# Kernel optimization log

Hardware: AMD Instinct MI355X
Metric: run time of the kernel (lower is better)

Reference implementation:

```python
import jax, jax.numpy as jnp
import numpy as np

B, L, D_MODEL = 8, 256, 256
D_STATE, D_INNER, DT_RANK, D_CONV = 16, 512, 16, 4


def _ln(x, g, b, eps):
    mu = x.mean(-1, keepdims=True)
    var = ((x - mu) ** 2).mean(-1, keepdims=True)
    return (x - mu) * jax.lax.rsqrt(var + eps) * g + b


def _ssm(x, W_in, conv_w, conv_b, W_x, W_dt, b_dt, A_log, Dp, W_out):
    # x: (B, L, D_MODEL) -- standard Mamba selective-scan block
    xz = x @ W_in                                  # (B,L,2*Di)
    xc, z = jnp.split(xz, 2, axis=-1)
    K = conv_w.shape[-1]
    xp = jnp.pad(xc, ((0, 0), (K - 1, 0), (0, 0)))  # causal depthwise conv
    xc = sum(xp[:, k:k + L, :] * conv_w[:, k] for k in range(K)) + conv_b
    xc = jax.nn.silu(xc)
    x_dbl = xc @ W_x                               # (B,L,R+2S)
    dt, Bm, Cm = jnp.split(x_dbl, [DT_RANK, DT_RANK + D_STATE], axis=-1)
    dt = jax.nn.softplus(dt @ W_dt + b_dt)         # (B,L,Di)
    A = -jnp.exp(A_log)                            # (Di,S)
    dA = jnp.exp(dt[..., None] * A)                # (B,L,Di,S)
    dBx = dt[..., None] * Bm[:, :, None, :] * xc[..., None]

    def step(h, inp):
        dA_t, dBx_t, C_t = inp
        h = dA_t * h + dBx_t                       # (B,Di,S)
        y = jnp.einsum('bds,bs->bd', h, C_t)
        return h, y

    h0 = jnp.zeros((xc.shape[0], D_INNER, D_STATE), xc.dtype)
    xs = (dA.transpose(1, 0, 2, 3), dBx.transpose(1, 0, 2, 3), Cm.transpose(1, 0, 2))
    _, ys = jax.lax.scan(step, h0, xs)             # (L,B,Di)
    y = ys.transpose(1, 0, 2) + xc * Dp
    y = y * jax.nn.silu(z)
    return y @ W_out


def _basic(x, ln_g, ln_b, ssm_params):
    # Basic_Block: ReLU(SSM(LN(x))) + x  (drop_path=0, attn_drop=0)
    return jax.nn.relu(_ssm(_ln(x, ln_g, ln_b, 1e-6), *ssm_params)) + x


def setup_inputs() -> dict:
    key = jax.random.key(0)
    ks = jax.random.split(key, 32)

    def n(k, shape, s=0.02):
        return jax.random.normal(k, shape, dtype=jnp.float32) * s

    inp = {}
    inp['x_spa'] = jax.random.normal(ks[0], (B, L, D_MODEL), dtype=jnp.float32)
    inp['x_spe'] = jax.random.normal(ks[1], (B, L, D_MODEL), dtype=jnp.float32)
    i = 2
    A_init = jnp.log(jnp.tile(jnp.arange(1, D_STATE + 1, dtype=jnp.float32), (D_INNER, 1)))
    for p in ('spa', 'spe'):
        inp[p + '_ln_g'] = jnp.ones((D_MODEL,), jnp.float32)
        inp[p + '_ln_b'] = jnp.zeros((D_MODEL,), jnp.float32)
        inp[p + '_W_in'] = n(ks[i], (D_MODEL, 2 * D_INNER)); i += 1
        inp[p + '_conv_w'] = n(ks[i], (D_INNER, D_CONV), 0.1); i += 1
        inp[p + '_conv_b'] = jnp.zeros((D_INNER,), jnp.float32)
        inp[p + '_W_x'] = n(ks[i], (D_INNER, DT_RANK + 2 * D_STATE)); i += 1
        inp[p + '_W_dt'] = n(ks[i], (DT_RANK, D_INNER), 0.1); i += 1
        inp[p + '_b_dt'] = n(ks[i], (D_INNER,), 0.1); i += 1
        inp[p + '_A_log'] = A_init
        inp[p + '_D'] = jnp.ones((D_INNER,), jnp.float32)
        inp[p + '_W_out'] = n(ks[i], (D_INNER, D_MODEL)); i += 1
    inp['sc_W'] = n(ks[i], (D_MODEL, D_MODEL)); i += 1
    inp['sc_b'] = jnp.zeros((D_MODEL,), jnp.float32)
    inp['sc_ln_g'] = jnp.ones((D_MODEL,), jnp.float32)
    inp['sc_ln_b'] = jnp.zeros((D_MODEL,), jnp.float32)
    inp['fusion_W'] = n(ks[i], (D_MODEL, D_MODEL))
    return inp


def reference(x_spa, x_spe,
              spa_ln_g, spa_ln_b, spa_W_in, spa_conv_w, spa_conv_b, spa_W_x,
              spa_W_dt, spa_b_dt, spa_A_log, spa_D, spa_W_out,
              spe_ln_g, spe_ln_b, spe_W_in, spe_conv_w, spe_conv_b, spe_W_x,
              spe_W_dt, spe_b_dt, spe_A_log, spe_D, spe_W_out,
              sc_W, sc_b, sc_ln_g, sc_ln_b, fusion_W):
    # shared shortcut: Linear + LayerNorm (eps=1e-5)
    ident_spa = _ln(x_spa @ sc_W + sc_b, sc_ln_g, sc_ln_b, 1e-5)
    ident_spe = _ln(x_spe @ sc_W + sc_b, sc_ln_g, sc_ln_b, 1e-5)
    spa_p = (spa_W_in, spa_conv_w, spa_conv_b, spa_W_x, spa_W_dt, spa_b_dt, spa_A_log, spa_D, spa_W_out)
    spe_p = (spe_W_in, spe_conv_w, spe_conv_b, spe_W_x, spe_W_dt, spe_b_dt, spe_A_log, spe_D, spe_W_out)
    a = _basic(x_spa, spa_ln_g, spa_ln_b, spa_p)
    e = _basic(x_spe, spe_ln_g, spe_ln_b, spe_p)
    # fusion gate: mean-pool both branches, Linear(no bias) + sigmoid, broadcast-mul
    fw = jax.nn.sigmoid(((a.mean(1) + e.mean(1)) * 0.5) @ fusion_W)[:, None, :]
    a = a * fw
    e = e * fw
    return (a + ident_spa, e + ident_spe)
```

## Files before the change

kernel.cpp:

```cpp
#include <hip/hip_runtime.h>
#include <hip/hip_bf16.h>
#include <math.h>

#define BD 8
#define LD 256
#define DM 256
#define DS 16
#define DI 512
#define RK 16

#define NROWS (2*BD*LD)
#define HALF_ROWS (BD*LD)

typedef __attribute__((ext_vector_type(8))) short bhalf8;
typedef __attribute__((ext_vector_type(4))) float f32x4;

__device__ __forceinline__ float siluf(float x){ return x / (1.f + __expf(-x)); }
__device__ __forceinline__ float softplusf(float x){
  return fmaxf(x, 0.f) + log1pf(__expf(-fabsf(x)));
}
__device__ __forceinline__ unsigned short f2bf(float f){
  __hip_bfloat16 h = __float2bfloat16(f);
  return *reinterpret_cast<unsigned short*>(&h);
}

__global__ __launch_bounds__(256) void k_transpose(
    const float* __restrict__ Wi_spa, const float* __restrict__ Wi_spe,
    const float* __restrict__ Wo_spa, const float* __restrict__ Wo_spe,
    const float* __restrict__ scW,
    const float* __restrict__ Wx_spa, const float* __restrict__ Wx_spe,
    unsigned short* __restrict__ Wt_i_spa, unsigned short* __restrict__ Wt_i_spe,
    unsigned short* __restrict__ Wt_o_spa, unsigned short* __restrict__ Wt_o_spe,
    unsigned short* __restrict__ scWt,
    unsigned short* __restrict__ Wxt_spa, unsigned short* __restrict__ Wxt_spe)
{
  __shared__ unsigned short tile[256][68];
  __shared__ float tile2[128][49];
  int b = blockIdx.x;
  int tid = threadIdx.x;
  if (b >= 52){
    int bb = b - 52;
    int branch = bb >> 2, chunk = bb & 3;
    int k0 = chunk*128;
    const float* Wx = branch ? Wx_spe : Wx_spa;
    unsigned short* Wxt = branch ? Wxt_spe : Wxt_spa;
    for (int i=tid; i<128*48; i+=256){
      int kk = i/48, c = i - kk*48;
      tile2[kk][c] = Wx[(k0+kk)*48 + c];
    }
    __syncthreads();
    for (int i=tid; i<64*128; i+=256){
      int cc = i >> 7, kk = i & 127;
      float v = (cc < 48) ? tile2[kk][cc] : 0.f;
      Wxt[cc*512 + k0 + kk] = f2bf(v);
    }
    return;
  }
  const float* W; unsigned short* Wt; int N, K, c0, k0;
  if (b < 32){
    int bb = b & 15;
    W  = (b < 16) ? Wi_spa  : Wi_spe;
    Wt = (b < 16) ? Wt_i_spa: Wt_i_spe;
    N = 1024; K = 256; c0 = (bb >> 2)*256; k0 = (bb & 3)*64;
  } else if (b < 48){
    int bb = b - 32; int h = bb >> 3; bb &= 7;
    W  = h ? Wo_spe  : Wo_spa;
    Wt = h ? Wt_o_spe: Wt_o_spa;
    N = 256; K = 512; c0 = 0; k0 = bb*64;
  } else {
    int bb = b - 48;
    W = scW; Wt = scWt;
    N = 256; K = 256; c0 = 0; k0 = bb*64;
  }
  int c = c0 + tid;
  #pragma unroll 8
  for (int kk=0; kk<64; kk++)
    tile[tid][kk] = f2bf(W[(k0+kk)*N + c]);
  __syncthreads();
  for (int p=0; p<16; p++){
    int i = tid + 256*p;
    int cl = i >> 4, kq = (i & 15)*4;
    uint2 v = *(const uint2*)&tile[cl][kq];
    *(uint2*)&Wt[(c0+cl)*K + k0 + kq] = v;
  }
}

__global__ __launch_bounds__(256) void k_lnwin(
    const float* __restrict__ x_spa, const float* __restrict__ x_spe,
    const float* __restrict__ g_spa, const float* __restrict__ b_spa,
    const float* __restrict__ g_spe, const float* __restrict__ b_spe,
    const unsigned short* __restrict__ Wt_spa, const unsigned short* __restrict__ Wt_spe,
    float* __restrict__ xc_raw, float* __restrict__ szout)
{
  __shared__ unsigned short At[16][264];
  __shared__ float red[16][16];
  __shared__ float mu[16], rs[16];
  int tid = threadIdx.x;
  int bi = blockIdx.x;
  int rg = bi >> 2, cg = bi & 3;
  int r0 = rg * 16;
  int branch = (r0 >= HALF_ROWS);
  const float* xb = branch ? x_spe : x_spa;
  const float* g  = branch ? g_spe : g_spa;
  const float* be = branch ? b_spe : b_spa;
  const unsigned short* Wt = branch ? Wt_spe : Wt_spa;
  int rr0 = branch ? r0 - HALF_ROWS : r0;

  {
    int row = tid >> 4, seg = tid & 15;
    const float* xp = xb + (rr0 + row)*DM + seg*16;
    float s = 0.f, s2 = 0.f;
    #pragma unroll
    for (int i=0;i<4;i++){
      float4 v = *(const float4*)(xp + i*4);
      s  += v.x+v.y+v.z+v.w;
      s2 += v.x*v.x + v.y*v.y + v.z*v.z + v.w*v.w;
    }
    red[row][seg] = s;
    __syncthreads();
    if (seg == 0){
      float t = 0.f;
      #pragma unroll
      for (int i=0;i<16;i++) t += red[row][i];
      mu[row] = t * (1.f/DM);
    }
    __syncthreads();
    float m = mu[row];
    float v2 = 0.f;
    #pragma unroll
    for (int i=0;i<4;i++){
      float4 v = *(const float4*)(xp + i*4);
      float dx=v.x-m, dy=v.y-m, dz=v.z-m, dw=v.w-m;
      v2 += dx*dx+dy*dy+dz*dz+dw*dw;
    }
    red[row][seg] = v2;
    __syncthreads();
    if (seg == 0){
      float t = 0.f;
      #pragma unroll
      for (int i=0;i<16;i++) t += red[row][i];
      rs[row] = rsqrtf(t*(1.f/DM) + 1e-6f);
    }
  }
  __syncthreads();
  for (int p=0;p<4;p++){
    int i4 = tid + 256*p;
    int r = i4 >> 6, kq = (i4 & 63)*4;
    float4 v  = *(const float4*)(xb + (rr0+r)*DM + kq);
    float4 gv = *(const float4*)(g + kq);
    float4 bv = *(const float4*)(be + kq);
    float m = mu[r], rv = rs[r];
    unsigned int lo = (unsigned int)f2bf((v.x-m)*rv*gv.x + bv.x)
                    | ((unsigned int)f2bf((v.y-m)*rv*gv.y + bv.y) << 16);
    unsigned int hi = (unsigned int)f2bf((v.z-m)*rv*gv.z + bv.z)
                    | ((unsigned int)f2bf((v.w-m)*rv*gv.w + bv.w) << 16);
    *(uint2*)&At[r][kq] = make_uint2(lo, hi);
  }
  __syncthreads();
  int w = tid >> 6, lane = tid & 63;
  int m16 = lane & 15, quad = lane >> 4;
  bhalf8 af[8];
  #pragma unroll
  for (int ks=0; ks<8; ks++)
    af[ks] = *(const bhalf8*)&At[m16][ks*32 + quad*8];
  f32x4 acc[4];
  #pragma unroll
  for (int ct=0; ct<4; ct++) acc[ct] = (f32x4)(0.f);
  const unsigned short* Wbw = Wt + (cg*256 + w*64)*256;
  #pragma unroll
  for (int ks=0; ks<8; ks++){
    #pragma unroll
    for (int ct=0; ct<4; ct++){
      bhalf8 bf = *(const bhalf8*)&Wbw[(ct*16 + m16)*256 + ks*32 + quad*8];
      acc[ct] = __builtin_amdgcn_mfma_f32_16x16x32_bf16(af[ks], bf, acc[ct], 0,0,0);
    }
  }
  bool isz = (cg >= 2);
  float* outp = isz ? szout : xc_raw;
  int cbase = (cg & 1)*256 + w*64;
  #pragma unroll
  for (int ct=0; ct<4; ct++){
    #pragma unroll
    for (int e=0;e<4;e++){
      int row = r0 + quad*4 + e;
      int col = cbase + ct*16 + m16;
      float v = acc[ct][e];
      if (isz) v = siluf(v);
      outp[row*DI + col] = v;
    }
  }
}

__global__ __launch_bounds__(256) void k_shortcut(
    const float* __restrict__ x_spa, const float* __restrict__ x_spe,
    const unsigned short* __restrict__ scWt, const float* __restrict__ sc_b,
    const float* __restrict__ ln_g, const float* __restrict__ ln_b,
    float* __restrict__ ident)
{
  __shared__ unsigned short At[16][264];
  __shared__ float Dt[16][260];
  __shared__ float red[16][16];
  __shared__ float mu[16], rs[16];
  int tid = threadIdx.x;
  int r0 = blockIdx.x * 16;
  int branch = (r0 >= HALF_ROWS);
  const float* xb = branch ? x_spe : x_spa;
  int rr0 = branch ? r0 - HALF_ROWS : r0;
  for (int p=0;p<4;p++){
    int i4 = tid + 256*p;
    int r = i4 >> 6, kq = (i4 & 63)*4;
    float4 v = *(const float4*)(xb + (rr0+r)*DM + kq);
    unsigned int lo = (unsigned int)f2bf(v.x) | ((unsigned int)f2bf(v.y) << 16);
    unsigned int hi = (unsigned int)f2bf(v.z) | ((unsigned int)f2bf(v.w) << 16);
    *(uint2*)&At[r][kq] = make_uint2(lo, hi);
  }
  __syncthreads();
  int w = tid >> 6, lane = tid & 63;
  int m16 = lane & 15, quad = lane >> 4;
  bhalf8 af[8];
  #pragma unroll
  for (int ks=0; ks<8; ks++)
    af[ks] = *(const bhalf8*)&At[m16][ks*32 + quad*8];
  f32x4 acc[4];
  #pragma unroll
  for (int ct=0; ct<4; ct++) acc[ct] = (f32x4)(0.f);
  const unsigned short* Wbw = scWt + (w*64)*256;
  #pragma unroll
  for (int ks=0; ks<8; ks++){
    #pragma unroll
    for (int ct=0; ct<4; ct++){
      bhalf8 bf = *(const bhalf8*)&Wbw[(ct*16 + m16)*256 + ks*32 + quad*8];
      acc[ct] = __builtin_amdgcn_mfma_f32_16x16x32_bf16(af[ks], bf, acc[ct], 0,0,0);
    }
  }
  #pragma unroll
  for (int ct=0; ct<4; ct++){
    #pragma unroll
    for (int e=0;e<4;e++){
      int row = quad*4 + e;
      int col = w*64 + ct*16 + m16;
      Dt[row][col] = acc[ct][e] + sc_b[col];
    }
  }
  __syncthreads();
  {
    int row = tid >> 4, seg = tid & 15;
    float s = 0.f, s2 = 0.f;
    #pragma unroll
    for (int i=0;i<4;i++){
      float4 v = *(const float4*)&Dt[row][seg*16 + i*4];
      s  += v.x+v.y+v.z+v.w;
      s2 += v.x*v.x + v.y*v.y + v.z*v.z + v.w*v.w;
    }
    red[row][seg] = s;
    __syncthreads();
    if (seg == 0){
      float t=0.f;
      #pragma unroll
      for (int i=0;i<16;i++) t += red[row][i];
      mu[row] = t * (1.f/DM);
    }
    __syncthreads();
    red[row][seg] = s2;
    __syncthreads();
    if (seg == 0){
      float t=0.f;
      #pragma unroll
      for (int i=0;i<16;i++) t += red[row][i];
      float m = mu[row];
      rs[row] = rsqrtf(t*(1.f/DM) - m*m + 1e-5f);
    }
  }
  __syncthreads();
  float gg = ln_g[tid], bb = ln_b[tid];
  #pragma unroll
  for (int r=0;r<16;r++)
    ident[(r0+r)*DM + tid] = (Dt[r][tid]-mu[r])*rs[r]*gg + bb;
}

__global__ __launch_bounds__(256) void k_conv(
    const float* __restrict__ cw_spa, const float* __restrict__ cb_spa,
    const float* __restrict__ cw_spe, const float* __restrict__ cb_spe,
    const float* __restrict__ xc_raw,
    float* __restrict__ xc, unsigned short* __restrict__ xcb)
{
  int tid = threadIdx.x;
  int r0 = blockIdx.x * 16;
  int branch = r0 >= HALF_ROWS;
  int l0 = r0 & (LD-1);
  const float* cw = branch ? cw_spe : cw_spa;
  const float* cb = branch ? cb_spe : cb_spa;
  int c = tid*2;
  float4 w0 = *(const float4*)(cw + 4*c);
  float4 w1 = *(const float4*)(cw + 4*(c+1));
  float2 bias = *(const float2*)(cb + c);
  float2 h0, h1, h2;
  if (l0 > 0){
    h0 = *(const float2*)(xc_raw + (r0-3)*DI + c);
    h1 = *(const float2*)(xc_raw + (r0-2)*DI + c);
    h2 = *(const float2*)(xc_raw + (r0-1)*DI + c);
  } else {
    h0 = make_float2(0.f,0.f); h1 = h0; h2 = h0;
  }
  #pragma unroll
  for (int r=0;r<16;r++){
    float2 cur = *(const float2*)(xc_raw + (r0+r)*DI + c);
    float vx = bias.x;
    vx = fmaf(h0.x, w0.x, vx); vx = fmaf(h1.x, w0.y, vx);
    vx = fmaf(h2.x, w0.z, vx); vx = fmaf(cur.x, w0.w, vx);
    float vy = bias.y;
    vy = fmaf(h0.y, w1.x, vy); vy = fmaf(h1.y, w1.y, vy);
    vy = fmaf(h2.y, w1.z, vy); vy = fmaf(cur.y, w1.w, vy);
    vx = siluf(vx); vy = siluf(vy);
    *(float2*)(xc + (r0+r)*DI + c) = make_float2(vx, vy);
    unsigned int pk = (unsigned int)f2bf(vx) | ((unsigned int)f2bf(vy) << 16);
    *(unsigned int*)&xcb[(r0+r)*DI + c] = pk;
    h0 = h1; h1 = h2; h2 = cur;
  }
}

__global__ __launch_bounds__(256) void k_xdbl(
    const unsigned short* __restrict__ xcb,
    const unsigned short* __restrict__ Wxt_spa, const unsigned short* __restrict__ Wxt_spe,
    const float* __restrict__ Wdt_spa, const float* __restrict__ bdt_spa,
    const float* __restrict__ Wdt_spe, const float* __restrict__ bdt_spe,
    float* __restrict__ dt, float* __restrict__ Bm, float* __restrict__ Cm)
{
  __shared__ unsigned short At[16][520];
  __shared__ float xdbl[16][18];
  int tid = threadIdx.x;
  int r0 = blockIdx.x * 16;
  int branch = r0 >= HALF_ROWS;
  const unsigned short* Wxt = branch ? Wxt_spe : Wxt_spa;
  const float* Wdt = branch ? Wdt_spe : Wdt_spa;
  const float* bdt = branch ? bdt_spe : bdt_spa;
  for (int p=0;p<4;p++){
    int i = tid + 256*p;
    int r = i >> 6, q = (i & 63)*8;
    *(uint4*)&At[r][q] = *(const uint4*)&xcb[(r0+r)*DI + q];
  }
  __syncthreads();
  int w = tid >> 6, lane = tid & 63;
  int m16 = lane & 15, quad = lane >> 4;
  f32x4 acc = (f32x4)(0.f);
  #pragma unroll
  for (int ks=0; ks<16; ks++){
    bhalf8 a = *(const bhalf8*)&At[m16][ks*32 + quad*8];
    bhalf8 bf = *(const bhalf8*)&Wxt[(w*16 + m16)*512 + ks*32 + quad*8];
    acc = __builtin_amdgcn_mfma_f32_16x16x32_bf16(a, bf, acc, 0,0,0);
  }
  #pragma unroll
  for (int e=0;e<4;e++){
    int row = quad*4 + e;
    float v = acc[e];
    if (w == 0)      xdbl[row][m16] = v;
    else if (w == 1) Bm[(r0+row)*DS + m16] = v;
    else if (w == 2) Cm[(r0+row)*DS + m16] = v;
  }
  __syncthreads();
  float wdt0[16], wdt1[16];
  #pragma unroll
  for (int j=0;j<16;j++){ wdt0[j]=Wdt[j*DI+tid]; wdt1[j]=Wdt[j*DI+tid+256]; }
  float b0 = bdt[tid], b1 = bdt[tid+256];
  #pragma unroll
  for (int r=0;r<16;r++){
    float a0=b0, a1=b1;
    #pragma unroll
    for (int j=0;j<16;j++){
      float xv = xdbl[r][j];
      a0 = fmaf(xv, wdt0[j], a0);
      a1 = fmaf(xv, wdt1[j], a1);
    }
    dt[(r0+r)*DI + tid]       = softplusf(a0);
    dt[(r0+r)*DI + tid + 256] = softplusf(a1);
  }
}

__global__ __launch_bounds__(256) void k_scan(
    const float* __restrict__ Alog_spa, const float* __restrict__ Dp_spa,
    const float* __restrict__ Alog_spe, const float* __restrict__ Dp_spe,
    const float* __restrict__ dt, const float* __restrict__ xc,
    const float* __restrict__ sz, const float* __restrict__ Bm,
    const float* __restrict__ Cm, float* __restrict__ y)
{
  __shared__ float ypbuf[16][260];
  __shared__ float Dsh[16];
  int tid = threadIdx.x;
  int bi = blockIdx.x;
  int branch = bi >> 8;
  int rem = bi & 255;
  int b = rem >> 5;
  int d0 = (rem & 31) * 16;
  const float* Alog = branch ? Alog_spe : Alog_spa;
  const float* Dp   = branch ? Dp_spe   : Dp_spa;
  int dg = tid >> 4, s = tid & 15;
  int d = d0 + dg;
  float A_ds = -__expf(Alog[d*DS + s]);
  if (tid < 16) Dsh[tid] = Dp[d0 + tid];
  int row0 = branch*HALF_ROWS + b*LD;
  int rli = tid >> 4, rdd = tid & 15;
  float h = 0.f;
  for (int c=0; c<16; c++){
    int rbase = row0 + c*16;
    float rdt[16], rxc[16], rB[16], rC[16];
    #pragma unroll
    for (int li=0; li<16; li++){
      rdt[li] = dt[(rbase+li)*DI + d];
      rxc[li] = xc[(rbase+li)*DI + d];
      rB[li]  = Bm[(rbase+li)*DS + s];
      rC[li]  = Cm[(rbase+li)*DS + s];
    }
    __syncthreads();
    #pragma unroll
    for (int li=0; li<16; li++){
      float dA = __expf(rdt[li] * A_ds);
      h = fmaf(dA, h, rdt[li] * rB[li] * rxc[li]);
      ypbuf[li][s*16 + ((dg + s) & 15)] = h * rC[li];
    }
    __syncthreads();
    float acc = 0.f;
    #pragma unroll
    for (int ss=0; ss<16; ss++)
      acc += ypbuf[rli][ss*16 + ((rdd + ss) & 15)];
    int grow = rbase + rli;
    float xcv = xc[grow*DI + d0 + rdd];
    float szv = sz[grow*DI + d0 + rdd];
    y[grow*DI + d0 + rdd] = fmaf(xcv, Dsh[rdd], acc) * szv;
  }
}

__global__ __launch_bounds__(256) void k_wout(
    const unsigned short* __restrict__ Wt_spa, const unsigned short* __restrict__ Wt_spe,
    const float* __restrict__ x_spa, const float* __restrict__ x_spe,
    const float* __restrict__ y, float* __restrict__ ae)
{
  __shared__ unsigned short At[16][520];
  int tid = threadIdx.x;
  int bi = blockIdx.x;
  int r0 = (bi >> 1) * 16;
  int ch = bi & 1;
  int branch = (r0 >= HALF_ROWS);
  const unsigned short* Wt = branch ? Wt_spe : Wt_spa;
  const float* xb = branch ? x_spe : x_spa;
  int rr0 = branch ? r0 - HALF_ROWS : r0;
  for (int p=0;p<8;p++){
    int i4 = tid + 256*p;
    int r = i4 >> 7, kq = (i4 & 127)*4;
    float4 v = *(const float4*)(y + (r0+r)*DI + kq);
    unsigned int lo = (unsigned int)f2bf(v.x) | ((unsigned int)f2bf(v.y) << 16);
    unsigned int hi = (unsigned int)f2bf(v.z) | ((unsigned int)f2bf(v.w) << 16);
    *(uint2*)&At[r][kq] = make_uint2(lo, hi);
  }
  __syncthreads();
  int w = tid >> 6, lane = tid & 63;
  int m16 = lane & 15, quad = lane >> 4;
  bhalf8 af[16];
  #pragma unroll
  for (int ks=0; ks<16; ks++)
    af[ks] = *(const bhalf8*)&At[m16][ks*32 + quad*8];
  f32x4 acc[2];
  #pragma unroll
  for (int ct=0; ct<2; ct++) acc[ct] = (f32x4)(0.f);
  const unsigned short* Wbw = Wt + (ch*128 + w*32)*512;
  #pragma unroll
  for (int ks=0; ks<16; ks++){
    #pragma unroll
    for (int ct=0; ct<2; ct++){
      bhalf8 bf = *(const bhalf8*)&Wbw[(ct*16 + m16)*512 + ks*32 + quad*8];
      acc[ct] = __builtin_amdgcn_mfma_f32_16x16x32_bf16(af[ks], bf, acc[ct], 0,0,0);
    }
  }
  #pragma unroll
  for (int ct=0; ct<2; ct++){
    #pragma unroll
    for (int e=0;e<4;e++){
      int row = quad*4 + e;
      int col = ch*128 + w*32 + ct*16 + m16;
      float v = fmaxf(acc[ct][e], 0.f) + xb[(rr0+row)*DM + col];
      ae[(r0+row)*DM + col] = v;
    }
  }
}

__global__ __launch_bounds__(256) void k_poolgate(const float* __restrict__ ae,
    const float* __restrict__ fW, float* __restrict__ fw)
{
  __shared__ float p[DM];
  int b=blockIdx.x, c=threadIdx.x;
  const float* a0 = ae + (b*LD)*DM + c;
  const float* a1 = ae + ((BD + b)*LD)*DM + c;
  float s=0.f;
  #pragma unroll 8
  for(int l=0;l<LD;l++) s += a0[l*DM] + a1[l*DM];
  p[c] = s * (0.5f/LD);
  __syncthreads();
  float a=0.f;
  for(int k=0;k<DM;k+=4){
    a = fmaf(p[k+0], fW[(k+0)*DM+c], a);
    a = fmaf(p[k+1], fW[(k+1)*DM+c], a);
    a = fmaf(p[k+2], fW[(k+2)*DM+c], a);
    a = fmaf(p[k+3], fW[(k+3)*DM+c], a);
  }
  fw[b*DM+c]=1.f/(1.f+__expf(-a));
}

__global__ __launch_bounds__(256) void k_final(const float* __restrict__ ae,
    const float* __restrict__ ident, const float* __restrict__ fw, float* __restrict__ out)
{
  int idx4 = blockIdx.x*256 + threadIdx.x;
  int row = idx4 >> 6;
  int b = (row >> 8) & 7;
  int c4 = (idx4 & 63) * 4;
  float4 av = *(const float4*)(ae + idx4*4);
  float4 iv = *(const float4*)(ident + idx4*4);
  float4 fv = *(const float4*)(fw + b*DM + c4);
  float4 o;
  o.x = fmaf(av.x, fv.x, iv.x);
  o.y = fmaf(av.y, fv.y, iv.y);
  o.z = fmaf(av.z, fv.z, iv.z);
  o.w = fmaf(av.w, fv.w, iv.w);
  *(float4*)(out + idx4*4) = o;
}

extern "C" void kernel_launch(void* const* d_in, const int* in_sizes, int n_in,
                              void* d_out, int out_size, void* d_ws, size_t ws_size,
                              hipStream_t stream) {
  const float* x_spa     = (const float*)d_in[0];
  const float* x_spe     = (const float*)d_in[1];
  const float* spa_ln_g  = (const float*)d_in[2];
  const float* spa_ln_b  = (const float*)d_in[3];
  const float* spa_W_in  = (const float*)d_in[4];
  const float* spa_cw    = (const float*)d_in[5];
  const float* spa_cb    = (const float*)d_in[6];
  const float* spa_W_x   = (const float*)d_in[7];
  const float* spa_W_dt  = (const float*)d_in[8];
  const float* spa_b_dt  = (const float*)d_in[9];
  const float* spa_A_log = (const float*)d_in[10];
  const float* spa_D     = (const float*)d_in[11];
  const float* spa_W_out = (const float*)d_in[12];
  const float* spe_ln_g  = (const float*)d_in[13];
  const float* spe_ln_b  = (const float*)d_in[14];
  const float* spe_W_in  = (const float*)d_in[15];
  const float* spe_cw    = (const float*)d_in[16];
  const float* spe_cb    = (const float*)d_in[17];
  const float* spe_W_x   = (const float*)d_in[18];
  const float* spe_W_dt  = (const float*)d_in[19];
  const float* spe_b_dt  = (const float*)d_in[20];
  const float* spe_A_log = (const float*)d_in[21];
  const float* spe_D     = (const float*)d_in[22];
  const float* spe_W_out = (const float*)d_in[23];
  const float* sc_W      = (const float*)d_in[24];
  const float* sc_b      = (const float*)d_in[25];
  const float* sc_ln_g   = (const float*)d_in[26];
  const float* sc_ln_b   = (const float*)d_in[27];
  const float* fusion_W  = (const float*)d_in[28];

  float* ws = (float*)d_ws;
  float* ident  = ws;
  float* xc_raw = ident  + NROWS*DM;
  float* sz     = xc_raw + NROWS*DI;
  float* xc     = sz     + NROWS*DI;
  float* dt     = xc     + NROWS*DI;
  float* Bm     = dt     + NROWS*DI;
  float* Cm     = Bm     + NROWS*DS;
  float* fw     = Cm     + NROWS*DS;
  unsigned short* Wt_i_spa = (unsigned short*)(fw + BD*DM);
  unsigned short* Wt_i_spe = Wt_i_spa + 1024*256;
  unsigned short* Wt_o_spa = Wt_i_spe + 1024*256;
  unsigned short* Wt_o_spe = Wt_o_spa + 256*512;
  unsigned short* scWt     = Wt_o_spe + 256*512;
  unsigned short* Wxt_spa  = scWt     + 256*256;
  unsigned short* Wxt_spe  = Wxt_spa  + 64*512;
  unsigned short* xcb      = Wxt_spe  + 64*512;

  float* out = (float*)d_out;

  k_transpose<<<60, 256, 0, stream>>>(spa_W_in, spe_W_in, spa_W_out, spe_W_out, sc_W,
                                      spa_W_x, spe_W_x,
                                      Wt_i_spa, Wt_i_spe, Wt_o_spa, Wt_o_spe, scWt,
                                      Wxt_spa, Wxt_spe);
  k_lnwin<<<1024, 256, 0, stream>>>(x_spa, x_spe, spa_ln_g, spa_ln_b, spe_ln_g, spe_ln_b,
                                    Wt_i_spa, Wt_i_spe, xc_raw, sz);
  k_conv<<<NROWS/16, 256, 0, stream>>>(spa_cw, spa_cb, spe_cw, spe_cb, xc_raw, xc, xcb);
  k_xdbl<<<NROWS/16, 256, 0, stream>>>(xcb, Wxt_spa, Wxt_spe,
                                       spa_W_dt, spa_b_dt, spe_W_dt, spe_b_dt,
                                       dt, Bm, Cm);
  float* y = xc_raw;
  k_scan<<<512, 256, 0, stream>>>(spa_A_log, spa_D, spe_A_log, spe_D, dt, xc, sz, Bm, Cm, y);
  k_shortcut<<<NROWS/16, 256, 0, stream>>>(x_spa, x_spe, scWt, sc_b, sc_ln_g, sc_ln_b, ident);
  float* ae = dt;
  k_wout<<<512, 256, 0, stream>>>(Wt_o_spa, Wt_o_spe, x_spa, x_spe, y, ae);
  k_poolgate<<<BD, 256, 0, stream>>>(ae, fusion_W, fw);
  k_final<<<NROWS*DM/1024, 256, 0, stream>>>(ae, ident, fw, out);
}
```

Before: 229.2 us.

## Fuse conv into x_dbl GEMM, stage scan inputs in LDS, pool via atomics

Merges the causal conv+SiLU kernel with the x_dbl projection so the bf16 activations go straight into shared memory instead of a global round trip. The scan now loads each chunk of dt/xc/sz/B/C cooperatively into LDS with float4 loads rather than per-thread strided reads. The mean pooling moves into the W_out epilogue using wave shuffles and atomicAdd, which replaces the 8-block pooling kernel that reread the whole activation. Atomics make the pooled sum order nondeterministic, and the scan picks up extra barriers.

```diff
diff --git a/kernel.cpp b/kernel.cpp
--- a/kernel.cpp
+++ b/kernel.cpp
@@ -32,12 +32,17 @@
     unsigned short* __restrict__ Wt_i_spa, unsigned short* __restrict__ Wt_i_spe,
     unsigned short* __restrict__ Wt_o_spa, unsigned short* __restrict__ Wt_o_spe,
     unsigned short* __restrict__ scWt,
-    unsigned short* __restrict__ Wxt_spa, unsigned short* __restrict__ Wxt_spe)
+    unsigned short* __restrict__ Wxt_spa, unsigned short* __restrict__ Wxt_spe,
+    float* __restrict__ pooled)
 {
   __shared__ unsigned short tile[256][68];
   __shared__ float tile2[128][49];
   int b = blockIdx.x;
   int tid = threadIdx.x;
+  if (b == 60){
+    for (int i=tid; i<BD*DM; i+=256) pooled[i] = 0.f;
+    return;
+  }
   if (b >= 52){
     int bb = b - 52;
     int branch = bb >> 2, chunk = bb & 3;
@@ -109,12 +114,11 @@
   {
     int row = tid >> 4, seg = tid & 15;
     const float* xp = xb + (rr0 + row)*DM + seg*16;
-    float s = 0.f, s2 = 0.f;
+    float s = 0.f;
     #pragma unroll
     for (int i=0;i<4;i++){
       float4 v = *(const float4*)(xp + i*4);
       s  += v.x+v.y+v.z+v.w;
-      s2 += v.x*v.x + v.y*v.y + v.z*v.z + v.w*v.w;
     }
     red[row][seg] = s;
     __syncthreads();
@@ -278,66 +282,55 @@
     ident[(r0+r)*DM + tid] = (Dt[r][tid]-mu[r])*rs[r]*gg + bb;
 }
 
-__global__ __launch_bounds__(256) void k_conv(
+__global__ __launch_bounds__(256) void k_convdbl(
     const float* __restrict__ cw_spa, const float* __restrict__ cb_spa,
     const float* __restrict__ cw_spe, const float* __restrict__ cb_spe,
     const float* __restrict__ xc_raw,
-    float* __restrict__ xc, unsigned short* __restrict__ xcb)
-{
+    const unsigned short* __restrict__ Wxt_spa, const unsigned short* __restrict__ Wxt_spe,
+    const float* __restrict__ Wdt_spa, const float* __restrict__ bdt_spa,
+    const float* __restrict__ Wdt_spe, const float* __restrict__ bdt_spe,
+    float* __restrict__ xc, float* __restrict__ dt,
+    float* __restrict__ Bm, float* __restrict__ Cm)
+{
+  __shared__ unsigned short At[16][520];
+  __shared__ float xdbl[16][18];
   int tid = threadIdx.x;
   int r0 = blockIdx.x * 16;
   int branch = r0 >= HALF_ROWS;
   int l0 = r0 & (LD-1);
   const float* cw = branch ? cw_spe : cw_spa;
   const float* cb = branch ? cb_spe : cb_spa;
-  int c = tid*2;
-  float4 w0 = *(const float4*)(cw + 4*c);
-  float4 w1 = *(const float4*)(cw + 4*(c+1));
-  float2 bias = *(const float2*)(cb + c);
-  float2 h0, h1, h2;
-  if (l0 > 0){
-    h0 = *(const float2*)(xc_raw + (r0-3)*DI + c);
-    h1 = *(const float2*)(xc_raw + (r0-2)*DI + c);
-    h2 = *(const float2*)(xc_raw + (r0-1)*DI + c);
-  } else {
-    h0 = make_float2(0.f,0.f); h1 = h0; h2 = h0;
-  }
-  #pragma unroll
-  for (int r=0;r<16;r++){
-    float2 cur = *(const float2*)(xc_raw + (r0+r)*DI + c);
-    float vx = bias.x;
-    vx = fmaf(h0.x, w0.x, vx); vx = fmaf(h1.x, w0.y, vx);
-    vx = fmaf(h2.x, w0.z, vx); vx = fmaf(cur.x, w0.w, vx);
-    float vy = bias.y;
-    vy = fmaf(h0.y, w1.x, vy); vy = fmaf(h1.y, w1.y, vy);
-    vy = fmaf(h2.y, w1.z, vy); vy = fmaf(cur.y, w1.w, vy);
-    vx = siluf(vx); vy = siluf(vy);
-    *(float2*)(xc + (r0+r)*DI + c) = make_float2(vx, vy);
-    unsigned int pk = (unsigned int)f2bf(vx) | ((unsigned int)f2bf(vy) << 16);
-    *(unsigned int*)&xcb[(r0+r)*DI + c] = pk;
-    h0 = h1; h1 = h2; h2 = cur;
-  }
-}
-
-__global__ __launch_bounds__(256) void k_xdbl(
-    const unsigned short* __restrict__ xcb,
-    const unsigned short* __restrict__ Wxt_spa, const unsigned short* __restrict__ Wxt_spe,
-    const float* __restrict__ Wdt_spa, const float* __restrict__ bdt_spa,
-    const float* __restrict__ Wdt_spe, const float* __restrict__ bdt_spe,
-    float* __restrict__ dt, float* __restrict__ Bm, float* __restrict__ Cm)
-{
-  __shared__ unsigned short At[16][520];
-  __shared__ float xdbl[16][18];
-  int tid = threadIdx.x;
-  int r0 = blockIdx.x * 16;
-  int branch = r0 >= HALF_ROWS;
   const unsigned short* Wxt = branch ? Wxt_spe : Wxt_spa;
   const float* Wdt = branch ? Wdt_spe : Wdt_spa;
   const float* bdt = branch ? bdt_spe : bdt_spa;
-  for (int p=0;p<4;p++){
-    int i = tid + 256*p;
-    int r = i >> 6, q = (i & 63)*8;
-    *(uint4*)&At[r][q] = *(const uint4*)&xcb[(r0+r)*DI + q];
+  {
+    int c = tid*2;
+    float4 w0 = *(const float4*)(cw + 4*c);
+    float4 w1 = *(const float4*)(cw + 4*(c+1));
+    float2 bias = *(const float2*)(cb + c);
+    float2 h0, h1, h2;
+    if (l0 > 0){
+      h0 = *(const float2*)(xc_raw + (r0-3)*DI + c);
+      h1 = *(const float2*)(xc_raw + (r0-2)*DI + c);
+      h2 = *(const float2*)(xc_raw + (r0-1)*DI + c);
+    } else {
+      h0 = make_float2(0.f,0.f); h1 = h0; h2 = h0;
+    }
+    #pragma unroll
+    for (int r=0;r<16;r++){
+      float2 cur = *(const float2*)(xc_raw + (r0+r)*DI + c);
+      float vx = bias.x;
+      vx = fmaf(h0.x, w0.x, vx); vx = fmaf(h1.x, w0.y, vx);
+      vx = fmaf(h2.x, w0.z, vx); vx = fmaf(cur.x, w0.w, vx);
+      float vy = bias.y;
+      vy = fmaf(h0.y, w1.x, vy); vy = fmaf(h1.y, w1.y, vy);
+      vy = fmaf(h2.y, w1.z, vy); vy = fmaf(cur.y, w1.w, vy);
+      vx = siluf(vx); vy = siluf(vy);
+      *(float2*)(xc + (r0+r)*DI + c) = make_float2(vx, vy);
+      unsigned int pk = (unsigned int)f2bf(vx) | ((unsigned int)f2bf(vy) << 16);
+      *(unsigned int*)&At[r][c] = pk;
+      h0 = h1; h1 = h2; h2 = cur;
+    }
   }
   __syncthreads();
   int w = tid >> 6, lane = tid & 63;
@@ -383,6 +376,7 @@
     const float* __restrict__ sz, const float* __restrict__ Bm,
     const float* __restrict__ Cm, float* __restrict__ y)
 {
+  __shared__ float dts[16][20], xcs[16][20], szs[16][20], Bs[16][20], Cs[16][20];
   __shared__ float ypbuf[16][260];
   __shared__ float Dsh[16];
   int tid = threadIdx.x;
@@ -402,37 +396,48 @@
   float h = 0.f;
   for (int c=0; c<16; c++){
     int rbase = row0 + c*16;
-    float rdt[16], rxc[16], rB[16], rC[16];
+    for (int idx=tid; idx<320; idx+=256){
+      int arr = idx >> 6;
+      int j = idx & 63;
+      int r = j >> 2, c4 = (j & 3)*4;
+      float4 v;
+      if      (arr == 0) v = *(const float4*)(dt + (rbase+r)*DI + d0 + c4);
+      else if (arr == 1) v = *(const float4*)(xc + (rbase+r)*DI + d0 + c4);
+      else if (arr == 2) v = *(const float4*)(sz + (rbase+r)*DI + d0 + c4);
+      else if (arr == 3) v = *(const float4*)(Bm + (rbase+r)*DS + c4);
+      else               v = *(const float4*)(Cm + (rbase+r)*DS + c4);
+      if      (arr == 0) *(float4*)&dts[r][c4] = v;
+      else if (arr == 1) *(float4*)&xcs[r][c4] = v;
+      else if (arr == 2) *(float4*)&szs[r][c4] = v;
+      else if (arr == 3) *(float4*)&Bs[r][c4]  = v;
+      else               *(float4*)&Cs[r][c4]  = v;
+    }
+    __syncthreads();
     #pragma unroll
     for (int li=0; li<16; li++){
-      rdt[li] = dt[(rbase+li)*DI + d];
-      rxc[li] = xc[(rbase+li)*DI + d];
-      rB[li]  = Bm[(rbase+li)*DS + s];
-      rC[li]  = Cm[(rbase+li)*DS + s];
-    }
-    __syncthreads();
-    #pragma unroll
-    for (int li=0; li<16; li++){
-      float dA = __expf(rdt[li] * A_ds);
-      h = fmaf(dA, h, rdt[li] * rB[li] * rxc[li]);
-      ypbuf[li][s*16 + ((dg + s) & 15)] = h * rC[li];
+      float dtv = dts[li][dg];
+      float xcv = xcs[li][dg];
+      float dA = __expf(dtv * A_ds);
+      h = fmaf(dA, h, dtv * Bs[li][s] * xcv);
+      ypbuf[li][s*16 + ((dg + s) & 15)] = h * Cs[li][s];
     }
     __syncthreads();
     float acc = 0.f;
     #pragma unroll
     for (int ss=0; ss<16; ss++)
       acc += ypbuf[rli][ss*16 + ((rdd + ss) & 15)];
-    int grow = rbase + rli;
-    float xcv = xc[grow*DI + d0 + rdd];
-    float szv = sz[grow*DI + d0 + rdd];
-    y[grow*DI + d0 + rdd] = fmaf(xcv, Dsh[rdd], acc) * szv;
+    float xcv = xcs[rli][rdd];
+    float szv = szs[rli][rdd];
+    y[(rbase+rli)*DI + d0 + rdd] = fmaf(xcv, Dsh[rdd], acc) * szv;
+    __syncthreads();
   }
 }
 
 __global__ __launch_bounds__(256) void k_wout(
     const unsigned short* __restrict__ Wt_spa, const unsigned short* __restrict__ Wt_spe,
     const float* __restrict__ x_spa, const float* __restrict__ x_spe,
-    const float* __restrict__ y, float* __restrict__ ae)
+    const float* __restrict__ y, float* __restrict__ ae,
+    float* __restrict__ pooled)
 {
   __shared__ unsigned short At[16][520];
   int tid = threadIdx.x;
@@ -470,6 +475,7 @@
       acc[ct] = __builtin_amdgcn_mfma_f32_16x16x32_bf16(af[ks], bf, acc[ct], 0,0,0);
     }
   }
+  float ps0 = 0.f, ps1 = 0.f;
   #pragma unroll
   for (int ct=0; ct<2; ct++){
     #pragma unroll
@@ -478,21 +484,24 @@
       int col = ch*128 + w*32 + ct*16 + m16;
       float v = fmaxf(acc[ct][e], 0.f) + xb[(rr0+row)*DM + col];
       ae[(r0+row)*DM + col] = v;
-    }
-  }
-}
-
-__global__ __launch_bounds__(256) void k_poolgate(const float* __restrict__ ae,
+      if (ct == 0) ps0 += v; else ps1 += v;
+    }
+  }
+  ps0 += __shfl_xor(ps0, 16, 64); ps0 += __shfl_xor(ps0, 32, 64);
+  ps1 += __shfl_xor(ps1, 16, 64); ps1 += __shfl_xor(ps1, 32, 64);
+  if (quad == 0){
+    int bidx = (r0 >> 8) & 7;
+    atomicAdd(&pooled[bidx*DM + ch*128 + w*32 + m16],      ps0);
+    atomicAdd(&pooled[bidx*DM + ch*128 + w*32 + 16 + m16], ps1);
+  }
+}
+
+__global__ __launch_bounds__(256) void k_gate(const float* __restrict__ pooled,
     const float* __restrict__ fW, float* __restrict__ fw)
 {
   __shared__ float p[DM];
   int b=blockIdx.x, c=threadIdx.x;
-  const float* a0 = ae + (b*LD)*DM + c;
-  const float* a1 = ae + ((BD + b)*LD)*DM + c;
-  float s=0.f;
-  #pragma unroll 8
-  for(int l=0;l<LD;l++) s += a0[l*DM] + a1[l*DM];
-  p[c] = s * (0.5f/LD);
+  p[c] = pooled[b*DM+c] * (0.5f/LD);
   __syncthreads();
   float a=0.f;
   for(int k=0;k<DM;k+=4){
@@ -563,7 +572,8 @@
   float* dt     = xc     + NROWS*DI;
   float* Bm     = dt     + NROWS*DI;
   float* Cm     = Bm     + NROWS*DS;
-  float* fw     = Cm     + NROWS*DS;
+  float* pooled = Cm     + NROWS*DS;
+  float* fw     = pooled + BD*DM;
   unsigned short* Wt_i_spa = (unsigned short*)(fw + BD*DM);
   unsigned short* Wt_i_spe = Wt_i_spa + 1024*256;
   unsigned short* Wt_o_spa = Wt_i_spe + 1024*256;
@@ -571,25 +581,24 @@
   unsigned short* scWt     = Wt_o_spe + 256*512;
   unsigned short* Wxt_spa  = scWt     + 256*256;
   unsigned short* Wxt_spe  = Wxt_spa  + 64*512;
-  unsigned short* xcb      = Wxt_spe  + 64*512;
 
   float* out = (float*)d_out;
 
-  k_transpose<<<60, 256, 0, stream>>>(spa_W_in, spe_W_in, spa_W_out, spe_W_out, sc_W,
+  k_transpose<<<61, 256, 0, stream>>>(spa_W_in, spe_W_in, spa_W_out, spe_W_out, sc_W,
                                       spa_W_x, spe_W_x,
                                       Wt_i_spa, Wt_i_spe, Wt_o_spa, Wt_o_spe, scWt,
-                                      Wxt_spa, Wxt_spe);
+                                      Wxt_spa, Wxt_spe, pooled);
   k_lnwin<<<1024, 256, 0, stream>>>(x_spa, x_spe, spa_ln_g, spa_ln_b, spe_ln_g, spe_ln_b,
                                     Wt_i_spa, Wt_i_spe, xc_raw, sz);
-  k_conv<<<NROWS/16, 256, 0, stream>>>(spa_cw, spa_cb, spe_cw, spe_cb, xc_raw, xc, xcb);
-  k_xdbl<<<NROWS/16, 256, 0, stream>>>(xcb, Wxt_spa, Wxt_spe,
-                                       spa_W_dt, spa_b_dt, spe_W_dt, spe_b_dt,
-                                       dt, Bm, Cm);
+  k_convdbl<<<NROWS/16, 256, 0, stream>>>(spa_cw, spa_cb, spe_cw, spe_cb, xc_raw,
+                                          Wxt_spa, Wxt_spe,
+                                          spa_W_dt, spa_b_dt, spe_W_dt, spe_b_dt,
+                                          xc, dt, Bm, Cm);
   float* y = xc_raw;
   k_scan<<<512, 256, 0, stream>>>(spa_A_log, spa_D, spe_A_log, spe_D, dt, xc, sz, Bm, Cm, y);
   k_shortcut<<<NROWS/16, 256, 0, stream>>>(x_spa, x_spe, scWt, sc_b, sc_ln_g, sc_ln_b, ident);
   float* ae = dt;
-  k_wout<<<512, 256, 0, stream>>>(Wt_o_spa, Wt_o_spe, x_spa, x_spe, y, ae);
-  k_poolgate<<<BD, 256, 0, stream>>>(ae, fusion_W, fw);
+  k_wout<<<512, 256, 0, stream>>>(Wt_o_spa, Wt_o_spe, x_spa, x_spe, y, ae, pooled);
+  k_gate<<<BD, 256, 0, stream>>>(pooled, fusion_W, fw);
   k_final<<<NROWS*DM/1024, 256, 0, stream>>>(ae, ident, fw, out);
 }
```

Result: faster. 215.3 us (-6.0%).
